# Kernel tuning notes

Measured on AMD Instinct MI355X. Metric: run time of the kernel, lower is better.

Reference implementation:

```python
import jax, jax.numpy as jnp
import numpy as np

DIM = 256; HEADS = 8; WS = 7; ALPHA = 0.5
HD = DIM // HEADS                      # head_dim = 32
GH = int(HEADS * ALPHA); LH = HEADS - GH   # 4 global / 4 local heads
GD = GH * HD; LD = LH * HD             # 128 / 128
HID = int(DIM * 4.0)                   # mlp hidden = 1024
SCALE = HD ** -0.5


def ln(x, g, b, eps=1e-5):
    m = jnp.mean(x, -1, keepdims=True)
    v = jnp.var(x, -1, keepdims=True)
    return (x - m) * jax.lax.rsqrt(v + eps) * g + b


def setup_inputs() -> dict:
    key = jax.random.key(0)
    ks = jax.random.split(key, 12)
    B, H, W = 4, 112, 112
    N = H * W
    def p(k, shape, s=0.02):
        return jax.random.normal(k, shape, jnp.float32) * s
    return {
        'x': jax.random.normal(ks[0], (B, N, DIM), jnp.float32),
        'x_reverse': jax.random.normal(ks[1], (B, N, DIM), jnp.float32),
        'g1': jnp.ones((DIM,), jnp.float32), 'b1': jnp.zeros((DIM,), jnp.float32),
        'g2': jnp.ones((DIM,), jnp.float32), 'b2': jnp.zeros((DIM,), jnp.float32),
        'Gq_w': p(ks[2], (DIM, GD)), 'Gq_b': jnp.zeros((GD,), jnp.float32),
        'Gkv_w': p(ks[3], (DIM, 2 * GD)), 'Gkv_b': jnp.zeros((2 * GD,), jnp.float32),
        'Gp_w': p(ks[4], (GD, GD)), 'Gp_b': jnp.zeros((GD,), jnp.float32),
        'Lq_w': p(ks[5], (DIM, LD)), 'Lq_b': jnp.zeros((LD,), jnp.float32),
        'Lkv_w': p(ks[6], (DIM, 2 * LD)), 'Lkv_b': jnp.zeros((2 * LD,), jnp.float32),
        'Lp_w': p(ks[7], (LD, LD)), 'Lp_b': jnp.zeros((LD,), jnp.float32),
        'fc1_w': p(ks[8], (DIM, HID)), 'fc1_b': jnp.zeros((HID,), jnp.float32),
        'dw_w': p(ks[9], (HID, 1, 3, 3), 0.05), 'dw_b': jnp.zeros((HID,), jnp.float32),
        'fc2_w': p(ks[10], (HID, DIM)), 'fc2_b': jnp.zeros((DIM,), jnp.float32),
        'H': 112, 'W': 112,
    }


def reference(x, x_reverse, g1, b1, g2, b2,
              Gq_w, Gq_b, Gkv_w, Gkv_b, Gp_w, Gp_b,
              Lq_w, Lq_b, Lkv_w, Lkv_b, Lp_w, Lp_b,
              fc1_w, fc1_b, dw_w, dw_b, fc2_w, fc2_b, H, W):
    B, N, C = x.shape
    assert H % WS == 0 and W % WS == 0  # shapes chosen so no padding branch
    xn = ln(x, g1, b1).reshape(B, H, W, C)
    xrn = ln(x_reverse, g1, b1).reshape(B, H, W, C)

    # ---- Global attention: queries from every pixel, kv from avg-pooled (ws x ws) grid
    q = (xn.reshape(B, N, C) @ Gq_w + Gq_b).reshape(B, N, GH, HD)
    pooled = xrn.reshape(B, H // WS, WS, W // WS, WS, C).mean(axis=(2, 4)).reshape(B, -1, C)
    kv = (pooled @ Gkv_w + Gkv_b).reshape(B, -1, 2, GH, HD)
    k, v = kv[:, :, 0], kv[:, :, 1]
    a = jax.nn.softmax(jnp.einsum('bnhd,bmhd->bhnm', q, k) * SCALE, axis=-1)
    g_out = jnp.einsum('bhnm,bmhd->bnhd', a, v).reshape(B, H, W, GD) @ Gp_w + Gp_b

    # ---- Local windowed attention (ws x ws non-overlapping windows)
    hg, wg = H // WS, W // WS
    TG, T = hg * wg, WS * WS
    def windows(t):
        return t.reshape(B, hg, WS, wg, WS, C).transpose(0, 1, 3, 2, 4, 5).reshape(B, TG, T, C)
    xw, xrw = windows(xn), windows(xrn)
    ql = (xw @ Lq_w + Lq_b).reshape(B, TG, T, LH, HD)
    kvl = (xrw @ Lkv_w + Lkv_b).reshape(B, TG, T, 2, LH, HD)
    kl, vl = kvl[:, :, :, 0], kvl[:, :, :, 1]
    al = jax.nn.softmax(jnp.einsum('bgqhd,bgkhd->bghqk', ql, kl) * SCALE, axis=-1)
    lo = jnp.einsum('bghqk,bgkhd->bgqhd', al, vl).reshape(B, hg, wg, WS, WS, LD)
    lo = lo.transpose(0, 1, 3, 2, 4, 5).reshape(B, H, W, LD) @ Lp_w + Lp_b

    x = x + jnp.concatenate([g_out, lo], axis=-1).reshape(B, N, C)

    # ---- DWMlp: fc1 -> depthwise 3x3 conv -> GELU -> fc2
    h = ln(x, g2, b2) @ fc1_w + fc1_b
    himg = h.reshape(B, H, W, HID).transpose(0, 3, 1, 2)
    himg = jax.lax.conv_general_dilated(
        himg, dw_w, (1, 1), 'SAME', feature_group_count=HID,
        dimension_numbers=('NCHW', 'OIHW', 'NCHW')) + dw_b[None, :, None, None]
    h = jax.nn.gelu(himg.reshape(B, HID, N).transpose(0, 2, 1), approximate=False)
    return x + (h @ fc2_w + fc2_b)
```

## Files before the change

### kernel.cpp

```cpp
#include <hip/hip_runtime.h>
#include <hip/hip_bf16.h>
#include <math.h>

typedef __hip_bfloat16 bf16;
typedef __attribute__((ext_vector_type(8))) short bf16x8;
typedef __attribute__((ext_vector_type(4))) float f32x4;

static constexpr int B_  = 4;
static constexpr int Hh  = 112, Ww = 112;
static constexpr int Nn  = Hh * Ww;
static constexpr int Cc  = 256;
static constexpr int M_  = B_ * Nn;
static constexpr int GH_ = 4;
static constexpr int GD_ = 128;
static constexpr int LD_ = 128;
static constexpr int HID_ = 1024;
static constexpr int TG_ = 256;
static constexpr int T__ = 49;
static constexpr float SCALE_ = 0.17677669529663687f;

__device__ __forceinline__ float toF(const bf16 v)  { return __bfloat162float(v); }
__device__ __forceinline__ float toF(const float v) { return v; }
__device__ __forceinline__ void st_out(float* p, float v) { *p = v; }
__device__ __forceinline__ void st_out(bf16* p, float v)  { *p = __float2bfloat16(v); }

__device__ __forceinline__ float erf_fast(float x) {
  float ax = __builtin_fabsf(x);
  float t  = __builtin_amdgcn_rcpf(fmaf(0.3275911f, ax, 1.0f));
  float p  = fmaf(t, 1.061405429f, -1.453152027f);
  p = fmaf(t, p, 1.421413741f);
  p = fmaf(t, p, -0.284496736f);
  p = fmaf(t, p, 0.254829592f);
  p = p * t;
  float r = fmaf(-p, __expf(-ax * ax), 1.0f);
  return copysignf(r, x);
}

__device__ __forceinline__ void gload_lds16(const bf16* g, bf16* l) {
  using gvoid = const __attribute__((address_space(1))) void;
  using lvoid = __attribute__((address_space(3))) void;
  __builtin_amdgcn_global_load_lds((gvoid*)g, (lvoid*)l, 16, 0, 0);
}

__device__ __forceinline__ int win_row_map(int r) {
  int b  = r / Nn;
  int rr = r - b * Nn;
  int g  = rr / T__;
  int t  = rr - g * T__;
  int gh = g >> 4, gw = g & 15;
  int i  = t / 7,  j  = t - i * 7;
  int n  = (gh * 7 + i) * Ww + gw * 7 + j;
  return b * Nn + n;
}

__global__ void guard_fill_kernel(float* out) {
  out[threadIdx.x + blockIdx.x * 256] = 1.0e6f;
}

__global__ __launch_bounds__(256) void convert_all_kernel(
    const float* __restrict__ s0, const float* __restrict__ s1,
    const float* __restrict__ s2, const float* __restrict__ s3,
    const float* __restrict__ s4, const float* __restrict__ s5,
    const float* __restrict__ s6, const float* __restrict__ s7,
    bf16* __restrict__ wt) {
  int idx = blockIdx.x * 256 + threadIdx.x;
  const float* W; int K, N, base;
  if      (idx < 32768)  { W = s0; K = 256;  N = 128;  base = 0; }
  else if (idx < 98304)  { W = s1; K = 256;  N = 256;  base = 32768; }
  else if (idx < 114688) { W = s2; K = 128;  N = 128;  base = 98304; }
  else if (idx < 147456) { W = s3; K = 256;  N = 128;  base = 114688; }
  else if (idx < 212992) { W = s4; K = 256;  N = 256;  base = 147456; }
  else if (idx < 229376) { W = s5; K = 128;  N = 128;  base = 212992; }
  else if (idx < 491520) { W = s6; K = 256;  N = 1024; base = 229376; }
  else                   { W = s7; K = 1024; N = 256;  base = 491520; }
  int loc = idx - base;
  int n = loc / K, k = loc - n * K;
  wt[idx] = __float2bfloat16(W[(size_t)k * N + n]);
}

__global__ __launch_bounds__(256) void ln_dual_kernel(const float* __restrict__ x,
                                                      const float* __restrict__ xr,
                                                      const float* __restrict__ g,
                                                      const float* __restrict__ bta,
                                                      bf16* __restrict__ xn,
                                                      bf16* __restrict__ xrn) {
  const int tid = threadIdx.x;
  const int grp = tid >> 5;
  const int sub = tid & 31;
  const int c0 = sub * 8;
  const int rowA = blockIdx.x * 16 + grp * 2;
  const int rowB = rowA + 1;
  const float* src = blockIdx.y ? xr : x;
  bf16* dst = blockIdx.y ? xrn : xn;
  const float* pA = src + (size_t)rowA * Cc + c0;
  const float* pB = src + (size_t)rowB * Cc + c0;
  float4 a0 = *(const float4*)(pA);
  float4 a1 = *(const float4*)(pA + 4);
  float4 b0 = *(const float4*)(pB);
  float4 b1 = *(const float4*)(pB + 4);
  float sA  = (a0.x + a0.y) + (a0.z + a0.w) + (a1.x + a1.y) + (a1.z + a1.w);
  float ssA = a0.x * a0.x + a0.y * a0.y + a0.z * a0.z + a0.w * a0.w
            + a1.x * a1.x + a1.y * a1.y + a1.z * a1.z + a1.w * a1.w;
  float sB  = (b0.x + b0.y) + (b0.z + b0.w) + (b1.x + b1.y) + (b1.z + b1.w);
  float ssB = b0.x * b0.x + b0.y * b0.y + b0.z * b0.z + b0.w * b0.w
            + b1.x * b1.x + b1.y * b1.y + b1.z * b1.z + b1.w * b1.w;
  #pragma unroll
  for (int off = 1; off < 32; off <<= 1) {
    sA  += __shfl_xor(sA, off);
    ssA += __shfl_xor(ssA, off);
    sB  += __shfl_xor(sB, off);
    ssB += __shfl_xor(ssB, off);
  }
  float meanA = sA * (1.0f / Cc);
  float varA  = ssA * (1.0f / Cc) - meanA * meanA;
  float rA = rsqrtf(varA + 1e-5f);
  float meanB = sB * (1.0f / Cc);
  float varB  = ssB * (1.0f / Cc) - meanB * meanB;
  float rB = rsqrtf(varB + 1e-5f);
  float4 gv0 = *(const float4*)(g + c0);
  float4 gv1 = *(const float4*)(g + c0 + 4);
  float4 bv0 = *(const float4*)(bta + c0);
  float4 bv1 = *(const float4*)(bta + c0 + 4);
  __align__(16) bf16 oA[8], oB[8];
  oA[0] = __float2bfloat16((a0.x - meanA) * rA * gv0.x + bv0.x);
  oA[1] = __float2bfloat16((a0.y - meanA) * rA * gv0.y + bv0.y);
  oA[2] = __float2bfloat16((a0.z - meanA) * rA * gv0.z + bv0.z);
  oA[3] = __float2bfloat16((a0.w - meanA) * rA * gv0.w + bv0.w);
  oA[4] = __float2bfloat16((a1.x - meanA) * rA * gv1.x + bv1.x);
  oA[5] = __float2bfloat16((a1.y - meanA) * rA * gv1.y + bv1.y);
  oA[6] = __float2bfloat16((a1.z - meanA) * rA * gv1.z + bv1.z);
  oA[7] = __float2bfloat16((a1.w - meanA) * rA * gv1.w + bv1.w);
  oB[0] = __float2bfloat16((b0.x - meanB) * rB * gv0.x + bv0.x);
  oB[1] = __float2bfloat16((b0.y - meanB) * rB * gv0.y + bv0.y);
  oB[2] = __float2bfloat16((b0.z - meanB) * rB * gv0.z + bv0.z);
  oB[3] = __float2bfloat16((b0.w - meanB) * rB * gv0.w + bv0.w);
  oB[4] = __float2bfloat16((b1.x - meanB) * rB * gv1.x + bv1.x);
  oB[5] = __float2bfloat16((b1.y - meanB) * rB * gv1.y + bv1.y);
  oB[6] = __float2bfloat16((b1.z - meanB) * rB * gv1.z + bv1.z);
  oB[7] = __float2bfloat16((b1.w - meanB) * rB * gv1.w + bv1.w);
  *(uint4*)(dst + (size_t)rowA * Cc + c0) = *(uint4*)oA;
  *(uint4*)(dst + (size_t)rowB * Cc + c0) = *(uint4*)oB;
}

__global__ __launch_bounds__(64) void pool_kernel(const bf16* __restrict__ xrn,
                                                  bf16* __restrict__ pooled) {
  const int lane = threadIdx.x;
  const int c0 = lane * 4;
  const int g  = blockIdx.x;
  const int b  = blockIdx.y;
  const int gh = g >> 4, gw = g & 15;
  float acc[4] = {};
  union U4 { uint2 u; bf16 e[4]; };
  #pragma unroll
  for (int i = 0; i < 7; i++)
    for (int j = 0; j < 7; j++) {
      int n = (gh * 7 + i) * Ww + gw * 7 + j;
      U4 r4;
      r4.u = *(const uint2*)(xrn + ((size_t)b * Nn + n) * Cc + c0);
      #pragma unroll
      for (int u = 0; u < 4; u++) acc[u] += toF(r4.e[u]);
    }
  bf16 o[4];
  #pragma unroll
  for (int u = 0; u < 4; u++) o[u] = __float2bfloat16(acc[u] * (1.0f / 49.0f));
  *(uint2*)(pooled + ((size_t)b * TG_ + g) * Cc + c0) = *(uint2*)o;
}

template <typename OutT, bool WIN_A, bool RES, int BK = 32>
__global__ __launch_bounds__(256) void mfma_gemm_kernel(const bf16* __restrict__ A,
                                                        const bf16* __restrict__ Wt,
                                                        const float* __restrict__ bias,
                                                        const float* __restrict__ res,
                                                        OutT* __restrict__ out,
                                                        int M, int N, int K) {
  __shared__ __align__(16) bf16 As[128 * BK];
  __shared__ __align__(16) bf16 Bs[128 * BK];
  constexpr int LPR = BK / 8;
  constexpr int RPI = 512 / BK;
  constexpr int NI  = BK / 16;
  const int tid = threadIdx.x;
  const int bm = blockIdx.y * 128, bn = blockIdx.x * 128;
  const int lane = tid & 63, w = tid >> 6;
  const int wm = (w >> 1) * 64, wn = (w & 1) * 64;

  const int rbase = w * 32 + (lane / LPR);
  const int kq    = (lane % LPR) * 8;
  const bf16* Ag[NI];
  const bf16* Bg[NI];
  bf16* Al[NI];
  bf16* Bl[NI];
  #pragma unroll
  for (int t = 0; t < NI; t++) {
    const int srow = rbase + t * RPI;
    const int ar = bm + srow;
    const int as = WIN_A ? win_row_map(ar) : ar;
    Ag[t] = A  + (size_t)as * K + kq;
    Al[t] = &As[srow * BK + kq];
    Bg[t] = Wt + (size_t)(bn + srow) * K + kq;
    Bl[t] = &Bs[srow * BK + kq];
  }

  f32x4 acc[4][4];
  #pragma unroll
  for (int i = 0; i < 4; i++)
    #pragma unroll
    for (int j = 0; j < 4; j++) acc[i][j] = (f32x4){0.f, 0.f, 0.f, 0.f};

  const int r16  = lane & 15;
  const int koct = (lane >> 4) * 8;
  const int mrow = wm + r16;
  const int nrow = wn + r16;

  for (int k0 = 0; k0 < K; k0 += BK) {
    #pragma unroll
    for (int t = 0; t < NI; t++) {
      gload_lds16(Ag[t] + k0, Al[t]);
      gload_lds16(Bg[t] + k0, Bl[t]);
    }
    __syncthreads();
    #pragma unroll
    for (int kk = 0; kk < BK / 32; kk++) {
      bf16x8 af[4], bfr[4];
      #pragma unroll
      for (int i = 0; i < 4; i++) af[i]  = *(const bf16x8*)&As[(mrow + i * 16) * BK + kk * 32 + koct];
      #pragma unroll
      for (int j = 0; j < 4; j++) bfr[j] = *(const bf16x8*)&Bs[(nrow + j * 16) * BK + kk * 32 + koct];
      #pragma unroll
      for (int i = 0; i < 4; i++)
        #pragma unroll
        for (int j = 0; j < 4; j++)
          acc[i][j] = __builtin_amdgcn_mfma_f32_16x16x32_bf16(af[i], bfr[j], acc[i][j], 0, 0, 0);
    }
    __syncthreads();
  }

  const int r0 = (lane >> 4) * 4;
  #pragma unroll
  for (int j = 0; j < 4; j++) {
    const int col = bn + wn + j * 16 + r16;
    const float bv = bias[col];
    #pragma unroll
    for (int i = 0; i < 4; i++) {
      const int rowb = bm + wm + i * 16 + r0;
      #pragma unroll
      for (int r = 0; r < 4; r++) {
        size_t ro = (size_t)(rowb + r) * N + col;
        float v = acc[i][j][r] + bv;
        if (RES) v += res[ro];
        st_out(out + ro, v);
      }
    }
  }
}

__global__ __launch_bounds__(256) void gattn_kernel(const bf16* __restrict__ q,
                                                    const bf16* __restrict__ kv,
                                                    bf16* __restrict__ out) {
  __shared__ __align__(16) bf16 Ks[256][40];
  __shared__ __align__(16) bf16 Vt[32][264];
  __shared__ __align__(16) bf16 Ps[4][32][40];
  const int tid = threadIdx.x;
  const int lane = tid & 63, w = tid >> 6;
  const int h = blockIdx.y, b = blockIdx.z;
  const int n0 = blockIdx.x * 128;
  const int r16 = lane & 15, oct = (lane >> 4) * 8;
  const bf16* kvb = kv + (size_t)b * TG_ * 256;

  {
    const int key = tid;
    const bf16* kp = kvb + (size_t)key * 256 + h * 32;
    *(uint4*)&Ks[key][0]  = *(const uint4*)(kp);
    *(uint4*)&Ks[key][8]  = *(const uint4*)(kp + 8);
    *(uint4*)&Ks[key][16] = *(const uint4*)(kp + 16);
    *(uint4*)&Ks[key][24] = *(const uint4*)(kp + 24);
    union { uint4 u[4]; bf16 e[32]; } vv;
    vv.u[0] = *(const uint4*)(kp + 128);
    vv.u[1] = *(const uint4*)(kp + 136);
    vv.u[2] = *(const uint4*)(kp + 144);
    vv.u[3] = *(const uint4*)(kp + 152);
    #pragma unroll
    for (int d = 0; d < 32; d++) Vt[d][key] = vv.e[d];
  }
  const size_t qbase0 = ((size_t)(b * Nn + n0 + w * 32 + r16)) * GD_ + h * 32 + oct;
  bf16x8 aq0 = *(const bf16x8*)(q + qbase0);
  bf16x8 aq1 = *(const bf16x8*)(q + qbase0 + (size_t)16 * GD_);
  __syncthreads();

  f32x4 rs0 = {0.f, 0.f, 0.f, 0.f}, rs1 = {0.f, 0.f, 0.f, 0.f};
  f32x4 ov[2][2];
  #pragma unroll
  for (int i = 0; i < 2; i++)
    #pragma unroll
    for (int dt = 0; dt < 2; dt++) ov[i][dt] = (f32x4){0.f, 0.f, 0.f, 0.f};

  for (int c0 = 0; c0 < 256; c0 += 32) {
    #pragma unroll
    for (int t = 0; t < 2; t++) {
      bf16x8 bk = *(const bf16x8*)&Ks[c0 + t * 16 + r16][oct];
      f32x4 s0 = __builtin_amdgcn_mfma_f32_16x16x32_bf16(aq0, bk, (f32x4){0.f,0.f,0.f,0.f}, 0, 0, 0);
      f32x4 s1 = __builtin_amdgcn_mfma_f32_16x16x32_bf16(aq1, bk, (f32x4){0.f,0.f,0.f,0.f}, 0, 0, 0);
      const int prow = (lane >> 4) * 4;
      const int pcol = t * 16 + r16;
      #pragma unroll
      for (int r = 0; r < 4; r++) {
        bf16 pb0 = __float2bfloat16(__expf(s0[r] * SCALE_));
        bf16 pb1 = __float2bfloat16(__expf(s1[r] * SCALE_));
        rs0[r] += toF(pb0);
        rs1[r] += toF(pb1);
        Ps[w][prow + r][pcol]      = pb0;
        Ps[w][16 + prow + r][pcol] = pb1;
      }
    }
    bf16x8 ap0 = *(const bf16x8*)&Ps[w][r16][oct];
    bf16x8 ap1 = *(const bf16x8*)&Ps[w][16 + r16][oct];
    #pragma unroll
    for (int dt = 0; dt < 2; dt++) {
      bf16x8 bv = *(const bf16x8*)&Vt[dt * 16 + r16][c0 + oct];
      ov[0][dt] = __builtin_amdgcn_mfma_f32_16x16x32_bf16(ap0, bv, ov[0][dt], 0, 0, 0);
      ov[1][dt] = __builtin_amdgcn_mfma_f32_16x16x32_bf16(ap1, bv, ov[1][dt], 0, 0, 0);
    }
  }
  #pragma unroll
  for (int off = 1; off < 16; off <<= 1) {
    #pragma unroll
    for (int r = 0; r < 4; r++) {
      rs0[r] += __shfl_xor(rs0[r], off);
      rs1[r] += __shfl_xor(rs1[r], off);
    }
  }
  const int orow0 = b * Nn + n0 + w * 32 + (lane >> 4) * 4;
  #pragma unroll
  for (int r = 0; r < 4; r++) {
    float inv0 = 1.0f / rs0[r];
    float inv1 = 1.0f / rs1[r];
    size_t ro0 = (size_t)(orow0 + r) * GD_ + h * 32;
    size_t ro1 = ro0 + (size_t)16 * GD_;
    #pragma unroll
    for (int dt = 0; dt < 2; dt++) {
      out[ro0 + dt * 16 + r16] = __float2bfloat16(ov[0][dt][r] * inv0);
      out[ro1 + dt * 16 + r16] = __float2bfloat16(ov[1][dt][r] * inv1);
    }
  }
}

__global__ __launch_bounds__(256) void lattn_kernel(const bf16* __restrict__ ql,
                                                    const bf16* __restrict__ kvl,
                                                    bf16* __restrict__ out) {
  __shared__ __align__(16) bf16 Ks[4][64][40];
  __shared__ __align__(16) bf16 Vt[4][32][72];
  __shared__ __align__(16) bf16 Ps[4][64][72];
  const int tid = threadIdx.x;
  const int lane = tid & 63, w = tid >> 6;
  const int g = blockIdx.x, b = blockIdx.y;
  const int r16 = lane & 15, oct = (lane >> 4) * 8;
  const size_t wbase = ((size_t)b * TG_ + g) * T__;

  for (int u = tid; u < T__ * 32; u += 256) {
    int m = u >> 5, c8 = u & 31;
    union { uint4 q4; bf16 e[8]; } ch;
    ch.q4 = *(const uint4*)(kvl + (wbase + m) * 256 + c8 * 8);
    if (c8 < 16) {
      int h = c8 >> 2, d0 = (c8 & 3) * 8;
      *(uint4*)&Ks[h][m][d0] = ch.q4;
    } else {
      int cv = c8 - 16;
      int h = cv >> 2, d0 = (cv & 3) * 8;
      #pragma unroll
      for (int e = 0; e < 8; e++) Vt[h][d0 + e][m] = ch.e[e];
    }
  }
  for (int z = tid; z < 4 * 32 * 15; z += 256) {
    int h = z / 480, rem = z - h * 480;
    int d = rem / 15, key = 49 + (rem - d * 15);
    Vt[h][d][key] = __float2bfloat16(0.f);
  }
  bf16x8 aq[4];
  #pragma unroll
  for (int i = 0; i < 4; i++) {
    int qr = 16 * i + r16;
    if (qr > 48) qr = 48;
    aq[i] = *(const bf16x8*)(ql + (wbase + qr) * LD_ + w * 32 + oct);
  }
  __syncthreads();

  f32x4 s[4][4];
  #pragma unroll
  for (int j = 0; j < 4; j++) {
    bf16x8 bk = *(const bf16x8*)&Ks[w][16 * j + r16][oct];
    #pragma unroll
    for (int i = 0; i < 4; i++)
      s[i][j] = __builtin_amdgcn_mfma_f32_16x16x32_bf16(aq[i], bk, (f32x4){0.f,0.f,0.f,0.f}, 0, 0, 0);
  }

  const int prow = (lane >> 4) * 4;
  float rs[4][4];
  #pragma unroll
  for (int i = 0; i < 4; i++) {
    #pragma unroll
    for (int r = 0; r < 4; r++) {
      float acc = 0.f;
      #pragma unroll
      for (int j = 0; j < 4; j++) {
        float p = __expf(s[i][j][r] * SCALE_);
        if (j == 3 && r16 != 0) p = 0.f;
        bf16 pb = __float2bfloat16(p);
        Ps[w][16 * i + prow + r][16 * j + r16] = pb;
        acc += toF(pb);
      }
      #pragma unroll
      for (int off = 1; off < 16; off <<= 1) acc += __shfl_xor(acc, off);
      rs[i][r] = acc;
    }
  }

  f32x4 ov[4][2];
  #pragma unroll
  for (int i = 0; i < 4; i++) {
    ov[i][0] = (f32x4){0.f, 0.f, 0.f, 0.f};
    ov[i][1] = (f32x4){0.f, 0.f, 0.f, 0.f};
  }
  #pragma unroll
  for (int kc = 0; kc < 2; kc++) {
    bf16x8 bv0 = *(const bf16x8*)&Vt[w][r16][kc * 32 + oct];
    bf16x8 bv1 = *(const bf16x8*)&Vt[w][16 + r16][kc * 32 + oct];
    #pragma unroll
    for (int i = 0; i < 4; i++) {
      bf16x8 ap = *(const bf16x8*)&Ps[w][16 * i + r16][kc * 32 + oct];
      ov[i][0] = __builtin_amdgcn_mfma_f32_16x16x32_bf16(ap, bv0, ov[i][0], 0, 0, 0);
      ov[i][1] = __builtin_amdgcn_mfma_f32_16x16x32_bf16(ap, bv1, ov[i][1], 0, 0, 0);
    }
  }

  #pragma unroll
  for (int i = 0; i < 4; i++) {
    #pragma unroll
    for (int r = 0; r < 4; r++) {
      int qr = 16 * i + prow + r;
      if (qr < T__) {
        float inv = 1.0f / rs[i][r];
        size_t o = (wbase + qr) * LD_ + w * 32;
        out[o + r16]      = __float2bfloat16(ov[i][0][r] * inv);
        out[o + 16 + r16] = __float2bfloat16(ov[i][1][r] * inv);
      }
    }
  }
}

__global__ __launch_bounds__(256) void combine_ln_kernel(const float* __restrict__ x,
                                                         const bf16* __restrict__ gout,
                                                         const bf16* __restrict__ lo_w,
                                                         const float* __restrict__ g2,
                                                         const float* __restrict__ b2,
                                                         float* __restrict__ xres,
                                                         bf16* __restrict__ xn2) {
  const int tid = threadIdx.x;
  const int row = blockIdx.x * 8 + (tid >> 5);
  const int sub = tid & 31;
  const int c0 = sub * 8;
  int b = row / Nn, n = row - b * Nn;
  int y = n / Ww, xx = n - y * Ww;
  int gh = y / 7, i = y - gh * 7;
  int gw = xx / 7, j = xx - gw * 7;
  size_t wrow = ((size_t)b * TG_ + gh * 16 + gw) * T__ + i * 7 + j;
  union U8 { uint4 u; bf16 e[8]; } r8;
  if (sub < 16) r8.u = *(const uint4*)(gout + (size_t)row * GD_ + c0);
  else          r8.u = *(const uint4*)(lo_w + wrow * LD_ + (c0 - 128));
  const float* xp = x + (size_t)row * Cc + c0;
  float4 v0 = *(const float4*)(xp);
  float4 v1 = *(const float4*)(xp + 4);
  v0.x += toF(r8.e[0]); v0.y += toF(r8.e[1]); v0.z += toF(r8.e[2]); v0.w += toF(r8.e[3]);
  v1.x += toF(r8.e[4]); v1.y += toF(r8.e[5]); v1.z += toF(r8.e[6]); v1.w += toF(r8.e[7]);
  *(float4*)(xres + (size_t)row * Cc + c0)     = v0;
  *(float4*)(xres + (size_t)row * Cc + c0 + 4) = v1;
  float s  = (v0.x + v0.y) + (v0.z + v0.w) + (v1.x + v1.y) + (v1.z + v1.w);
  float ss = v0.x * v0.x + v0.y * v0.y + v0.z * v0.z + v0.w * v0.w
           + v1.x * v1.x + v1.y * v1.y + v1.z * v1.z + v1.w * v1.w;
  #pragma unroll
  for (int off = 1; off < 32; off <<= 1) {
    s  += __shfl_xor(s, off);
    ss += __shfl_xor(ss, off);
  }
  float mean = s * (1.0f / Cc);
  float var  = ss * (1.0f / Cc) - mean * mean;
  float r = rsqrtf(var + 1e-5f);
  float4 gv0 = *(const float4*)(g2 + c0);
  float4 gv1 = *(const float4*)(g2 + c0 + 4);
  float4 bv0 = *(const float4*)(b2 + c0);
  float4 bv1 = *(const float4*)(b2 + c0 + 4);
  __align__(16) bf16 o[8];
  o[0] = __float2bfloat16((v0.x - mean) * r * gv0.x + bv0.x);
  o[1] = __float2bfloat16((v0.y - mean) * r * gv0.y + bv0.y);
  o[2] = __float2bfloat16((v0.z - mean) * r * gv0.z + bv0.z);
  o[3] = __float2bfloat16((v0.w - mean) * r * gv0.w + bv0.w);
  o[4] = __float2bfloat16((v1.x - mean) * r * gv1.x + bv1.x);
  o[5] = __float2bfloat16((v1.y - mean) * r * gv1.y + bv1.y);
  o[6] = __float2bfloat16((v1.z - mean) * r * gv1.z + bv1.z);
  o[7] = __float2bfloat16((v1.w - mean) * r * gv1.w + bv1.w);
  *(uint4*)(xn2 + (size_t)row * Cc + c0) = *(uint4*)o;
}

static constexpr int TW_ = 14;
__global__ __launch_bounds__(256, 4) void dwconv_gelu_kernel(const bf16* __restrict__ h1,
                                                             const float* __restrict__ w,
                                                             const float* __restrict__ bias,
                                                             bf16* __restrict__ h2) {
  const int tid = threadIdx.x;
  const int c0 = tid * 4;
  const int img = blockIdx.z;
  const int y0  = blockIdx.y * 2;
  const int xt  = blockIdx.x * TW_;
  const size_t ibase = (size_t)img * Nn * HID_;

  float wreg[9][4], breg[4];
  #pragma unroll
  for (int u = 0; u < 4; u++) {
    breg[u] = bias[c0 + u];
    #pragma unroll
    for (int t = 0; t < 9; t++) wreg[t][u] = w[(c0 + u) * 9 + t];
  }

  const bf16* rowp[4];
  bool rok[4];
  #pragma unroll
  for (int r = 0; r < 4; r++) {
    int yy = y0 - 1 + r;
    rok[r] = (yy >= 0 && yy < Hh);
    rowp[r] = h1 + ibase + (size_t)(rok[r] ? yy : 0) * Ww * HID_ + c0;
  }

  float wa[4][4], wb[4][4], wc[4][4];
  union U4 { ushort2 u2[2]; bf16 e[4]; };
  auto loadcol = [&](int xcol, float v[4][4]) {
    if (xcol < 0 || xcol >= Ww) {
      #pragma unroll
      for (int r = 0; r < 4; r++)
        #pragma unroll
        for (int u = 0; u < 4; u++) v[r][u] = 0.f;
      return;
    }
    #pragma unroll
    for (int r = 0; r < 4; r++) {
      if (rok[r]) {
        U4 raw;
        *(uint2*)&raw = *(const uint2*)(rowp[r] + (size_t)xcol * HID_);
        #pragma unroll
        for (int u = 0; u < 4; u++) v[r][u] = toF(raw.e[u]);
      } else {
        #pragma unroll
        for (int u = 0; u < 4; u++) v[r][u] = 0.f;
      }
    }
  };
  loadcol(xt - 1, wa);
  loadcol(xt, wb);

  for (int xx = 0; xx < TW_; xx++) {
    const int x = xt + xx;
    loadcol(x + 1, wc);
    #pragma unroll
    for (int p = 0; p < 2; p++) {
      bf16 res[4];
      #pragma unroll
      for (int u = 0; u < 4; u++) {
        float a = breg[u];
        a = fmaf(wa[p + 0][u], wreg[0][u], a);
        a = fmaf(wb[p + 0][u], wreg[1][u], a);
        a = fmaf(wc[p + 0][u], wreg[2][u], a);
        a = fmaf(wa[p + 1][u], wreg[3][u], a);
        a = fmaf(wb[p + 1][u], wreg[4][u], a);
        a = fmaf(wc[p + 1][u], wreg[5][u], a);
        a = fmaf(wa[p + 2][u], wreg[6][u], a);
        a = fmaf(wb[p + 2][u], wreg[7][u], a);
        a = fmaf(wc[p + 2][u], wreg[8][u], a);
        float gl = 0.5f * a * (1.0f + erf_fast(a * 0.7071067811865475f));
        res[u] = __float2bfloat16(gl);
      }
      *(uint2*)(h2 + ibase + (size_t)((y0 + p) * Ww + x) * HID_ + c0) = *(uint2*)res;
    }
    #pragma unroll
    for (int r = 0; r < 4; r++)
      #pragma unroll
      for (int u = 0; u < 4; u++) { wa[r][u] = wb[r][u]; wb[r][u] = wc[r][u]; }
  }
}

extern "C" void kernel_launch(void* const* d_in, const int* in_sizes, int n_in,
                              void* d_out, int out_size, void* d_ws, size_t ws_size,
                              hipStream_t stream) {
  const float* x     = (const float*)d_in[0];
  const float* xrev  = (const float*)d_in[1];
  const float* g1    = (const float*)d_in[2];
  const float* b1    = (const float*)d_in[3];
  const float* g2    = (const float*)d_in[4];
  const float* b2    = (const float*)d_in[5];
  const float* Gq_w  = (const float*)d_in[6];
  const float* Gq_b  = (const float*)d_in[7];
  const float* Gkv_w = (const float*)d_in[8];
  const float* Gkv_b = (const float*)d_in[9];
  const float* Gp_w  = (const float*)d_in[10];
  const float* Gp_b  = (const float*)d_in[11];
  const float* Lq_w  = (const float*)d_in[12];
  const float* Lq_b  = (const float*)d_in[13];
  const float* Lkv_w = (const float*)d_in[14];
  const float* Lkv_b = (const float*)d_in[15];
  const float* Lp_w  = (const float*)d_in[16];
  const float* Lp_b  = (const float*)d_in[17];
  const float* fc1_w = (const float*)d_in[18];
  const float* fc1_b = (const float*)d_in[19];
  const float* dw_w  = (const float*)d_in[20];
  const float* dw_b  = (const float*)d_in[21];
  const float* fc2_w = (const float*)d_in[22];
  const float* fc2_b = (const float*)d_in[23];

  const size_t E_GQ = 256 * 128, E_GKV = 256 * 256, E_GP = 128 * 128;
  const size_t E_LQ = 256 * 128, E_LKV = 256 * 256, E_LP = 128 * 128;
  const size_t E_F1 = 256 * 1024, E_F2 = 1024 * 256;
  char* ws = (char*)d_ws;
  bf16* Gq_t  = (bf16*)ws;
  bf16* Gkv_t = Gq_t  + E_GQ;
  bf16* Gp_t  = Gkv_t + E_GKV;
  bf16* Lq_t  = Gp_t  + E_GP;
  bf16* Lkv_t = Lq_t  + E_LQ;
  bf16* Lp_t  = Lkv_t + E_LKV;
  bf16* f1_t  = Lp_t  + E_LP;
  bf16* f2_t  = f1_t  + E_F1;
  const size_t WT_ELEMS = E_GQ + E_GKV + E_GP + E_LQ + E_LKV + E_LP + E_F1 + E_F2;
  const size_t WT_BYTES = WT_ELEMS * 2;

  const size_t SZ_ROW2 = (size_t)M_ * Cc * 2;
  const size_t SZ_HALF = (size_t)M_ * 128 * 2;
  const size_t SZ_POOL = (size_t)B_ * TG_ * Cc * 2;
  const size_t SZ_KVG  = (size_t)B_ * TG_ * 256 * 2;
  const size_t SZ_H    = (size_t)(2 * Nn) * HID_ * 2;
  char* arena = ws + WT_BYTES;
  bf16* S1 = (bf16*)(arena);
  bf16* S2 = (bf16*)(arena + SZ_ROW2);
  bf16* S3 = (bf16*)(arena + 2 * SZ_ROW2);
  bf16* S4 = (bf16*)(arena + 2 * SZ_ROW2 + SZ_HALF);
  bf16* S5 = (bf16*)(arena + 2 * SZ_ROW2 + 2 * SZ_HALF);
  bf16* poolb = (bf16*)(arena + 2 * SZ_ROW2 + 3 * SZ_HALF);
  bf16* kvG   = (bf16*)(arena + 2 * SZ_ROW2 + 3 * SZ_HALF + SZ_POOL);
  const size_t ARENA_A = 2 * SZ_ROW2 + 3 * SZ_HALF + SZ_POOL + SZ_KVG;
  bf16* xn2 = S1;
  bf16* h1  = (bf16*)(arena + SZ_ROW2);
  bf16* h2  = (bf16*)(arena + SZ_ROW2 + SZ_H);
  const size_t ARENA_B = SZ_ROW2 + 2 * SZ_H;

  float* out  = (float*)d_out;
  float* xres = (float*)d_out;
  const size_t NEED = WT_BYTES + (ARENA_A > ARENA_B ? ARENA_A : ARENA_B);
  if (ws_size < NEED) {
    guard_fill_kernel<<<16, 256, 0, stream>>>(out);
    return;
  }

  bf16* xn = S1;  bf16* xrn = S2;  bf16* qbuf = S3;  bf16* gattn = S4;  bf16* gout = S5;
  bf16* kvl = S1; bf16* lo_w = S2; bf16* qlb  = S3;  bf16* lattn = S4;

  convert_all_kernel<<<2944, 256, 0, stream>>>(Gq_w, Gkv_w, Gp_w, Lq_w, Lkv_w, Lp_w,
                                               fc1_w, fc2_w, (bf16*)ws);
  ln_dual_kernel<<<dim3(M_ / 16, 2), 256, 0, stream>>>(x, xrev, g1, b1, xn, xrn);
  pool_kernel<<<dim3(TG_, B_), 64, 0, stream>>>(xrn, poolb);
  mfma_gemm_kernel<bf16, false, false><<<dim3(1, M_ / 128), 256, 0, stream>>>(
      xn, Gq_t, Gq_b, nullptr, qbuf, M_, 128, 256);
  mfma_gemm_kernel<bf16, false, false><<<dim3(2, 8), 256, 0, stream>>>(
      poolb, Gkv_t, Gkv_b, nullptr, kvG, 1024, 256, 256);
  gattn_kernel<<<dim3(Nn / 128, GH_, B_), 256, 0, stream>>>(qbuf, kvG, gattn);
  mfma_gemm_kernel<bf16, false, false><<<dim3(1, M_ / 128), 256, 0, stream>>>(
      gattn, Gp_t, Gp_b, nullptr, gout, M_, 128, 128);
  mfma_gemm_kernel<bf16, true, false><<<dim3(1, M_ / 128), 256, 0, stream>>>(
      xn, Lq_t, Lq_b, nullptr, qlb, M_, 128, 256);
  mfma_gemm_kernel<bf16, true, false><<<dim3(2, M_ / 128), 256, 0, stream>>>(
      xrn, Lkv_t, Lkv_b, nullptr, kvl, M_, 256, 256);
  lattn_kernel<<<dim3(TG_, B_), 256, 0, stream>>>(qlb, kvl, lattn);
  mfma_gemm_kernel<bf16, false, false><<<dim3(1, M_ / 128), 256, 0, stream>>>(
      lattn, Lp_t, Lp_b, nullptr, lo_w, M_, 128, 128);
  combine_ln_kernel<<<M_ / 8, 256, 0, stream>>>(x, gout, lo_w, g2, b2, xres, xn2);
  for (int half = 0; half < 2; half++) {
    const size_t r0 = (size_t)half * 2 * Nn;
    mfma_gemm_kernel<bf16, false, false, 64><<<dim3(8, (2 * Nn) / 128), 256, 0, stream>>>(
        xn2 + r0 * Cc, f1_t, fc1_b, nullptr, h1, 2 * Nn, 1024, 256);
    dwconv_gelu_kernel<<<dim3(Ww / TW_, Hh / 2, 2), 256, 0, stream>>>(h1, dw_w, dw_b, h2);
    mfma_gemm_kernel<float, false, true><<<dim3(2, (2 * Nn) / 128), 256, 0, stream>>>(
        h2, f2_t, fc2_b, xres + r0 * Cc, out + r0 * Cc, 2 * Nn, 256, 1024);
  }
}
```

Before: 537.9 us.

## Merge global/local q and projection GEMMs, drop window-order buffers

Concatenates the global and local query weights into one 256-wide GEMM and packs both output projections into a block-diagonal 256x256 weight, so one GEMM covers each pair. Local attention now gathers its window rows directly from pixel-ordered buffers, which removes the window-remapped GEMM loads and the remapped reads in combine. The LayerNorm kernel is also reshaped to one row per wavefront. This cuts kernel launches and intermediate traffic, but the block-diagonal projection does twice the FLOPs, and local attention loads become strided gathers.

```diff
diff --git a/kernel.cpp b/kernel.cpp
--- a/kernel.cpp
+++ b/kernel.cpp
@@ -12,8 +12,6 @@
 static constexpr int Cc  = 256;
 static constexpr int M_  = B_ * Nn;
 static constexpr int GH_ = 4;
-static constexpr int GD_ = 128;
-static constexpr int LD_ = 128;
 static constexpr int HID_ = 1024;
 static constexpr int TG_ = 256;
 static constexpr int T__ = 49;
@@ -42,40 +40,49 @@
   __builtin_amdgcn_global_load_lds((gvoid*)g, (lvoid*)l, 16, 0, 0);
 }
 
-__device__ __forceinline__ int win_row_map(int r) {
-  int b  = r / Nn;
-  int rr = r - b * Nn;
-  int g  = rr / T__;
-  int t  = rr - g * T__;
-  int gh = g >> 4, gw = g & 15;
-  int i  = t / 7,  j  = t - i * 7;
-  int n  = (gh * 7 + i) * Ww + gw * 7 + j;
-  return b * Nn + n;
-}
-
 __global__ void guard_fill_kernel(float* out) {
   out[threadIdx.x + blockIdx.x * 256] = 1.0e6f;
 }
 
 __global__ __launch_bounds__(256) void convert_all_kernel(
-    const float* __restrict__ s0, const float* __restrict__ s1,
-    const float* __restrict__ s2, const float* __restrict__ s3,
-    const float* __restrict__ s4, const float* __restrict__ s5,
-    const float* __restrict__ s6, const float* __restrict__ s7,
+    const float* __restrict__ gq, const float* __restrict__ lq,
+    const float* __restrict__ gkv, const float* __restrict__ lkv,
+    const float* __restrict__ gp, const float* __restrict__ lp,
+    const float* __restrict__ f1, const float* __restrict__ f2,
     bf16* __restrict__ wt) {
   int idx = blockIdx.x * 256 + threadIdx.x;
-  const float* W; int K, N, base;
-  if      (idx < 32768)  { W = s0; K = 256;  N = 128;  base = 0; }
-  else if (idx < 98304)  { W = s1; K = 256;  N = 256;  base = 32768; }
-  else if (idx < 114688) { W = s2; K = 128;  N = 128;  base = 98304; }
-  else if (idx < 147456) { W = s3; K = 256;  N = 128;  base = 114688; }
-  else if (idx < 212992) { W = s4; K = 256;  N = 256;  base = 147456; }
-  else if (idx < 229376) { W = s5; K = 128;  N = 128;  base = 212992; }
-  else if (idx < 491520) { W = s6; K = 256;  N = 1024; base = 229376; }
-  else                   { W = s7; K = 1024; N = 256;  base = 491520; }
-  int loc = idx - base;
-  int n = loc / K, k = loc - n * K;
-  wt[idx] = __float2bfloat16(W[(size_t)k * N + n]);
+  float v;
+  if (idx < 32768) {
+    int n = idx / 256, k = idx - n * 256;
+    v = gq[(size_t)k * 128 + n];
+  } else if (idx < 65536) {
+    int loc = idx - 32768;
+    int n = loc / 256, k = loc - n * 256;
+    v = lq[(size_t)k * 128 + n];
+  } else if (idx < 131072) {
+    int loc = idx - 65536;
+    int n = loc / 256, k = loc - n * 256;
+    v = gkv[(size_t)k * 256 + n];
+  } else if (idx < 196608) {
+    int loc = idx - 131072;
+    int n = loc / 256, k = loc - n * 256;
+    v = lkv[(size_t)k * 256 + n];
+  } else if (idx < 262144) {
+    int loc = idx - 196608;
+    int n = loc >> 8, k = loc & 255;
+    if (n < 128 && k < 128)       v = gp[(size_t)k * 128 + n];
+    else if (n >= 128 && k >= 128) v = lp[(size_t)(k - 128) * 128 + (n - 128)];
+    else                           v = 0.f;
+  } else if (idx < 524288) {
+    int loc = idx - 262144;
+    int n = loc / 256, k = loc - n * 256;
+    v = f1[(size_t)k * 1024 + n];
+  } else {
+    int loc = idx - 524288;
+    int n = loc / 1024, k = loc - n * 1024;
+    v = f2[(size_t)k * 256 + n];
+  }
+  wt[idx] = __float2bfloat16(v);
 }
 
 __global__ __launch_bounds__(256) void ln_dual_kernel(const float* __restrict__ x,
@@ -85,61 +92,30 @@
                                                       bf16* __restrict__ xn,
                                                       bf16* __restrict__ xrn) {
   const int tid = threadIdx.x;
-  const int grp = tid >> 5;
-  const int sub = tid & 31;
-  const int c0 = sub * 8;
-  const int rowA = blockIdx.x * 16 + grp * 2;
-  const int rowB = rowA + 1;
+  const int row = blockIdx.x * 4 + (tid >> 6);
+  const int lane = tid & 63;
+  const int c0 = lane * 4;
   const float* src = blockIdx.y ? xr : x;
   bf16* dst = blockIdx.y ? xrn : xn;
-  const float* pA = src + (size_t)rowA * Cc + c0;
-  const float* pB = src + (size_t)rowB * Cc + c0;
-  float4 a0 = *(const float4*)(pA);
-  float4 a1 = *(const float4*)(pA + 4);
-  float4 b0 = *(const float4*)(pB);
-  float4 b1 = *(const float4*)(pB + 4);
-  float sA  = (a0.x + a0.y) + (a0.z + a0.w) + (a1.x + a1.y) + (a1.z + a1.w);
-  float ssA = a0.x * a0.x + a0.y * a0.y + a0.z * a0.z + a0.w * a0.w
-            + a1.x * a1.x + a1.y * a1.y + a1.z * a1.z + a1.w * a1.w;
-  float sB  = (b0.x + b0.y) + (b0.z + b0.w) + (b1.x + b1.y) + (b1.z + b1.w);
-  float ssB = b0.x * b0.x + b0.y * b0.y + b0.z * b0.z + b0.w * b0.w
-            + b1.x * b1.x + b1.y * b1.y + b1.z * b1.z + b1.w * b1.w;
-  #pragma unroll
-  for (int off = 1; off < 32; off <<= 1) {
-    sA  += __shfl_xor(sA, off);
-    ssA += __shfl_xor(ssA, off);
-    sB  += __shfl_xor(sB, off);
-    ssB += __shfl_xor(ssB, off);
-  }
-  float meanA = sA * (1.0f / Cc);
-  float varA  = ssA * (1.0f / Cc) - meanA * meanA;
-  float rA = rsqrtf(varA + 1e-5f);
-  float meanB = sB * (1.0f / Cc);
-  float varB  = ssB * (1.0f / Cc) - meanB * meanB;
-  float rB = rsqrtf(varB + 1e-5f);
-  float4 gv0 = *(const float4*)(g + c0);
-  float4 gv1 = *(const float4*)(g + c0 + 4);
-  float4 bv0 = *(const float4*)(bta + c0);
-  float4 bv1 = *(const float4*)(bta + c0 + 4);
-  __align__(16) bf16 oA[8], oB[8];
-  oA[0] = __float2bfloat16((a0.x - meanA) * rA * gv0.x + bv0.x);
-  oA[1] = __float2bfloat16((a0.y - meanA) * rA * gv0.y + bv0.y);
-  oA[2] = __float2bfloat16((a0.z - meanA) * rA * gv0.z + bv0.z);
-  oA[3] = __float2bfloat16((a0.w - meanA) * rA * gv0.w + bv0.w);
-  oA[4] = __float2bfloat16((a1.x - meanA) * rA * gv1.x + bv1.x);
-  oA[5] = __float2bfloat16((a1.y - meanA) * rA * gv1.y + bv1.y);
-  oA[6] = __float2bfloat16((a1.z - meanA) * rA * gv1.z + bv1.z);
-  oA[7] = __float2bfloat16((a1.w - meanA) * rA * gv1.w + bv1.w);
-  oB[0] = __float2bfloat16((b0.x - meanB) * rB * gv0.x + bv0.x);
-  oB[1] = __float2bfloat16((b0.y - meanB) * rB * gv0.y + bv0.y);
-  oB[2] = __float2bfloat16((b0.z - meanB) * rB * gv0.z + bv0.z);
-  oB[3] = __float2bfloat16((b0.w - meanB) * rB * gv0.w + bv0.w);
-  oB[4] = __float2bfloat16((b1.x - meanB) * rB * gv1.x + bv1.x);
-  oB[5] = __float2bfloat16((b1.y - meanB) * rB * gv1.y + bv1.y);
-  oB[6] = __float2bfloat16((b1.z - meanB) * rB * gv1.z + bv1.z);
-  oB[7] = __float2bfloat16((b1.w - meanB) * rB * gv1.w + bv1.w);
-  *(uint4*)(dst + (size_t)rowA * Cc + c0) = *(uint4*)oA;
-  *(uint4*)(dst + (size_t)rowB * Cc + c0) = *(uint4*)oB;
+  float4 v = *(const float4*)(src + (size_t)row * Cc + c0);
+  float s  = v.x + v.y + v.z + v.w;
+  float ss = v.x * v.x + v.y * v.y + v.z * v.z + v.w * v.w;
+  #pragma unroll
+  for (int off = 1; off < 64; off <<= 1) {
+    s  += __shfl_xor(s, off);
+    ss += __shfl_xor(ss, off);
+  }
+  float mean = s * (1.0f / Cc);
+  float var  = ss * (1.0f / Cc) - mean * mean;
+  float r = rsqrtf(var + 1e-5f);
+  float4 gv = *(const float4*)(g + c0);
+  float4 bv = *(const float4*)(bta + c0);
+  bf16 o[4];
+  o[0] = __float2bfloat16((v.x - mean) * r * gv.x + bv.x);
+  o[1] = __float2bfloat16((v.y - mean) * r * gv.y + bv.y);
+  o[2] = __float2bfloat16((v.z - mean) * r * gv.z + bv.z);
+  o[3] = __float2bfloat16((v.w - mean) * r * gv.w + bv.w);
+  *(uint2*)(dst + (size_t)row * Cc + c0) = *(uint2*)o;
 }
 
 __global__ __launch_bounds__(64) void pool_kernel(const bf16* __restrict__ xrn,
@@ -166,10 +142,11 @@
   *(uint2*)(pooled + ((size_t)b * TG_ + g) * Cc + c0) = *(uint2*)o;
 }
 
-template <typename OutT, bool WIN_A, bool RES, int BK = 32>
+template <typename OutT, bool RES, int BK = 32>
 __global__ __launch_bounds__(256) void mfma_gemm_kernel(const bf16* __restrict__ A,
                                                         const bf16* __restrict__ Wt,
                                                         const float* __restrict__ bias,
+                                                        const float* __restrict__ bias2,
                                                         const float* __restrict__ res,
                                                         OutT* __restrict__ out,
                                                         int M, int N, int K) {
@@ -192,9 +169,7 @@
   #pragma unroll
   for (int t = 0; t < NI; t++) {
     const int srow = rbase + t * RPI;
-    const int ar = bm + srow;
-    const int as = WIN_A ? win_row_map(ar) : ar;
-    Ag[t] = A  + (size_t)as * K + kq;
+    Ag[t] = A  + (size_t)(bm + srow) * K + kq;
     Al[t] = &As[srow * BK + kq];
     Bg[t] = Wt + (size_t)(bn + srow) * K + kq;
     Bl[t] = &Bs[srow * BK + kq];
@@ -238,7 +213,7 @@
   #pragma unroll
   for (int j = 0; j < 4; j++) {
     const int col = bn + wn + j * 16 + r16;
-    const float bv = bias[col];
+    const float bv = (bias2 && col >= 128) ? bias2[col - 128] : bias[col];
     #pragma unroll
     for (int i = 0; i < 4; i++) {
       const int rowb = bm + wm + i * 16 + r0;
@@ -281,9 +256,9 @@
     #pragma unroll
     for (int d = 0; d < 32; d++) Vt[d][key] = vv.e[d];
   }
-  const size_t qbase0 = ((size_t)(b * Nn + n0 + w * 32 + r16)) * GD_ + h * 32 + oct;
+  const size_t qbase0 = ((size_t)(b * Nn + n0 + w * 32 + r16)) * 256 + h * 32 + oct;
   bf16x8 aq0 = *(const bf16x8*)(q + qbase0);
-  bf16x8 aq1 = *(const bf16x8*)(q + qbase0 + (size_t)16 * GD_);
+  bf16x8 aq1 = *(const bf16x8*)(q + qbase0 + (size_t)16 * 256);
   __syncthreads();
 
   f32x4 rs0 = {0.f, 0.f, 0.f, 0.f}, rs1 = {0.f, 0.f, 0.f, 0.f};
@@ -333,8 +308,8 @@
   for (int r = 0; r < 4; r++) {
     float inv0 = 1.0f / rs0[r];
     float inv1 = 1.0f / rs1[r];
-    size_t ro0 = (size_t)(orow0 + r) * GD_ + h * 32;
-    size_t ro1 = ro0 + (size_t)16 * GD_;
+    size_t ro0 = (size_t)(orow0 + r) * 256 + h * 32;
+    size_t ro1 = ro0 + (size_t)16 * 256;
     #pragma unroll
     for (int dt = 0; dt < 2; dt++) {
       out[ro0 + dt * 16 + r16] = __float2bfloat16(ov[0][dt][r] * inv0);
@@ -352,13 +327,16 @@
   const int tid = threadIdx.x;
   const int lane = tid & 63, w = tid >> 6;
   const int g = blockIdx.x, b = blockIdx.y;
+  const int gh = g >> 4, gw = g & 15;
   const int r16 = lane & 15, oct = (lane >> 4) * 8;
-  const size_t wbase = ((size_t)b * TG_ + g) * T__;
+  const int nw0 = (gh * 7) * Ww + gw * 7;
 
   for (int u = tid; u < T__ * 32; u += 256) {
     int m = u >> 5, c8 = u & 31;
+    int im = m / 7, jm = m - im * 7;
+    int nm = nw0 + im * Ww + jm;
     union { uint4 q4; bf16 e[8]; } ch;
-    ch.q4 = *(const uint4*)(kvl + (wbase + m) * 256 + c8 * 8);
+    ch.q4 = *(const uint4*)(kvl + ((size_t)b * Nn + nm) * 256 + c8 * 8);
     if (c8 < 16) {
       int h = c8 >> 2, d0 = (c8 & 3) * 8;
       *(uint4*)&Ks[h][m][d0] = ch.q4;
@@ -379,7 +357,9 @@
   for (int i = 0; i < 4; i++) {
     int qr = 16 * i + r16;
     if (qr > 48) qr = 48;
-    aq[i] = *(const bf16x8*)(ql + (wbase + qr) * LD_ + w * 32 + oct);
+    int iq = qr / 7, jq = qr - iq * 7;
+    int nq = nw0 + iq * Ww + jq;
+    aq[i] = *(const bf16x8*)(ql + ((size_t)b * Nn + nq) * 256 + 128 + w * 32 + oct);
   }
   __syncthreads();
 
@@ -438,7 +418,9 @@
       int qr = 16 * i + prow + r;
       if (qr < T__) {
         float inv = 1.0f / rs[i][r];
-        size_t o = (wbase + qr) * LD_ + w * 32;
+        int iq = qr / 7, jq = qr - iq * 7;
+        int nq = nw0 + iq * Ww + jq;
+        size_t o = ((size_t)b * Nn + nq) * 256 + 128 + w * 32;
         out[o + r16]      = __float2bfloat16(ov[i][0][r] * inv);
         out[o + 16 + r16] = __float2bfloat16(ov[i][1][r] * inv);
       }
@@ -447,8 +429,7 @@
 }
 
 __global__ __launch_bounds__(256) void combine_ln_kernel(const float* __restrict__ x,
-                                                         const bf16* __restrict__ gout,
-                                                         const bf16* __restrict__ lo_w,
+                                                         const bf16* __restrict__ proj,
                                                          const float* __restrict__ g2,
                                                          const float* __restrict__ b2,
                                                          float* __restrict__ xres,
@@ -457,14 +438,8 @@
   const int row = blockIdx.x * 8 + (tid >> 5);
   const int sub = tid & 31;
   const int c0 = sub * 8;
-  int b = row / Nn, n = row - b * Nn;
-  int y = n / Ww, xx = n - y * Ww;
-  int gh = y / 7, i = y - gh * 7;
-  int gw = xx / 7, j = xx - gw * 7;
-  size_t wrow = ((size_t)b * TG_ + gh * 16 + gw) * T__ + i * 7 + j;
   union U8 { uint4 u; bf16 e[8]; } r8;
-  if (sub < 16) r8.u = *(const uint4*)(gout + (size_t)row * GD_ + c0);
-  else          r8.u = *(const uint4*)(lo_w + wrow * LD_ + (c0 - 128));
+  r8.u = *(const uint4*)(proj + (size_t)row * 256 + c0);
   const float* xp = x + (size_t)row * Cc + c0;
   float4 v0 = *(const float4*)(xp);
   float4 v1 = *(const float4*)(xp + 4);
@@ -612,35 +587,33 @@
   const float* fc2_w = (const float*)d_in[22];
   const float* fc2_b = (const float*)d_in[23];
 
-  const size_t E_GQ = 256 * 128, E_GKV = 256 * 256, E_GP = 128 * 128;
-  const size_t E_LQ = 256 * 128, E_LKV = 256 * 256, E_LP = 128 * 128;
-  const size_t E_F1 = 256 * 1024, E_F2 = 1024 * 256;
+  const size_t E_QW = 256 * 256;
+  const size_t E_GKV = 256 * 256;
+  const size_t E_LKV = 256 * 256;
+  const size_t E_PJ = 256 * 256;
+  const size_t E_F1 = 1024 * 256, E_F2 = 256 * 1024;
   char* ws = (char*)d_ws;
-  bf16* Gq_t  = (bf16*)ws;
-  bf16* Gkv_t = Gq_t  + E_GQ;
-  bf16* Gp_t  = Gkv_t + E_GKV;
-  bf16* Lq_t  = Gp_t  + E_GP;
-  bf16* Lkv_t = Lq_t  + E_LQ;
-  bf16* Lp_t  = Lkv_t + E_LKV;
-  bf16* f1_t  = Lp_t  + E_LP;
+  bf16* QW_t  = (bf16*)ws;
+  bf16* Gkv_t = QW_t  + E_QW;
+  bf16* Lkv_t = Gkv_t + E_GKV;
+  bf16* PJ_t  = Lkv_t + E_LKV;
+  bf16* f1_t  = PJ_t  + E_PJ;
   bf16* f2_t  = f1_t  + E_F1;
-  const size_t WT_ELEMS = E_GQ + E_GKV + E_GP + E_LQ + E_LKV + E_LP + E_F1 + E_F2;
+  const size_t WT_ELEMS = E_QW + E_GKV + E_LKV + E_PJ + E_F1 + E_F2;
   const size_t WT_BYTES = WT_ELEMS * 2;
 
   const size_t SZ_ROW2 = (size_t)M_ * Cc * 2;
-  const size_t SZ_HALF = (size_t)M_ * 128 * 2;
   const size_t SZ_POOL = (size_t)B_ * TG_ * Cc * 2;
   const size_t SZ_KVG  = (size_t)B_ * TG_ * 256 * 2;
   const size_t SZ_H    = (size_t)(2 * Nn) * HID_ * 2;
   char* arena = ws + WT_BYTES;
-  bf16* S1 = (bf16*)(arena);
-  bf16* S2 = (bf16*)(arena + SZ_ROW2);
-  bf16* S3 = (bf16*)(arena + 2 * SZ_ROW2);
-  bf16* S4 = (bf16*)(arena + 2 * SZ_ROW2 + SZ_HALF);
-  bf16* S5 = (bf16*)(arena + 2 * SZ_ROW2 + 2 * SZ_HALF);
-  bf16* poolb = (bf16*)(arena + 2 * SZ_ROW2 + 3 * SZ_HALF);
-  bf16* kvG   = (bf16*)(arena + 2 * SZ_ROW2 + 3 * SZ_HALF + SZ_POOL);
-  const size_t ARENA_A = 2 * SZ_ROW2 + 3 * SZ_HALF + SZ_POOL + SZ_KVG;
+  bf16* S1       = (bf16*)(arena);
+  bf16* S2       = (bf16*)(arena + SZ_ROW2);
+  bf16* q_cat    = (bf16*)(arena + 2 * SZ_ROW2);
+  bf16* attn_cat = (bf16*)(arena + 3 * SZ_ROW2);
+  bf16* poolb    = (bf16*)(arena + 4 * SZ_ROW2);
+  bf16* kvG      = (bf16*)(arena + 4 * SZ_ROW2 + SZ_POOL);
+  const size_t ARENA_A = 4 * SZ_ROW2 + SZ_POOL + SZ_KVG;
   bf16* xn2 = S1;
   bf16* h1  = (bf16*)(arena + SZ_ROW2);
   bf16* h2  = (bf16*)(arena + SZ_ROW2 + SZ_H);
@@ -654,34 +627,29 @@
     return;
   }
 
-  bf16* xn = S1;  bf16* xrn = S2;  bf16* qbuf = S3;  bf16* gattn = S4;  bf16* gout = S5;
-  bf16* kvl = S1; bf16* lo_w = S2; bf16* qlb  = S3;  bf16* lattn = S4;
-
-  convert_all_kernel<<<2944, 256, 0, stream>>>(Gq_w, Gkv_w, Gp_w, Lq_w, Lkv_w, Lp_w,
+  bf16* xn = S1;  bf16* xrn = S2;  bf16* kvl = S1;  bf16* proj = q_cat;
+
+  convert_all_kernel<<<3072, 256, 0, stream>>>(Gq_w, Lq_w, Gkv_w, Lkv_w, Gp_w, Lp_w,
                                                fc1_w, fc2_w, (bf16*)ws);
-  ln_dual_kernel<<<dim3(M_ / 16, 2), 256, 0, stream>>>(x, xrev, g1, b1, xn, xrn);
+  ln_dual_kernel<<<dim3(M_ / 4, 2), 256, 0, stream>>>(x, xrev, g1, b1, xn, xrn);
   pool_kernel<<<dim3(TG_, B_), 64, 0, stream>>>(xrn, poolb);
-  mfma_gemm_kernel<bf16, false, false><<<dim3(1, M_ / 128), 256, 0, stream>>>(
-      xn, Gq_t, Gq_b, nullptr, qbuf, M_, 128, 256);
-  mfma_gemm_kernel<bf16, false, false><<<dim3(2, 8), 256, 0, stream>>>(
-      poolb, Gkv_t, Gkv_b, nullptr, kvG, 1024, 256, 256);
-  gattn_kernel<<<dim3(Nn / 128, GH_, B_), 256, 0, stream>>>(qbuf, kvG, gattn);
-  mfma_gemm_kernel<bf16, false, false><<<dim3(1, M_ / 128), 256, 0, stream>>>(
-      gattn, Gp_t, Gp_b, nullptr, gout, M_, 128, 128);
-  mfma_gemm_kernel<bf16, true, false><<<dim3(1, M_ / 128), 256, 0, stream>>>(
-      xn, Lq_t, Lq_b, nullptr, qlb, M_, 128, 256);
-  mfma_gemm_kernel<bf16, true, false><<<dim3(2, M_ / 128), 256, 0, stream>>>(
-      xrn, Lkv_t, Lkv_b, nullptr, kvl, M_, 256, 256);
-  lattn_kernel<<<dim3(TG_, B_), 256, 0, stream>>>(qlb, kvl, lattn);
-  mfma_gemm_kernel<bf16, false, false><<<dim3(1, M_ / 128), 256, 0, stream>>>(
-      lattn, Lp_t, Lp_b, nullptr, lo_w, M_, 128, 128);
-  combine_ln_kernel<<<M_ / 8, 256, 0, stream>>>(x, gout, lo_w, g2, b2, xres, xn2);
+  mfma_gemm_kernel<bf16, false><<<dim3(2, M_ / 128), 256, 0, stream>>>(
+      xn, QW_t, Gq_b, Lq_b, nullptr, q_cat, M_, 256, 256);
+  mfma_gemm_kernel<bf16, false><<<dim3(2, M_ / 128), 256, 0, stream>>>(
+      xrn, Lkv_t, Lkv_b, nullptr, nullptr, kvl, M_, 256, 256);
+  mfma_gemm_kernel<bf16, false><<<dim3(2, 8), 256, 0, stream>>>(
+      poolb, Gkv_t, Gkv_b, nullptr, nullptr, kvG, 1024, 256, 256);
+  gattn_kernel<<<dim3(Nn / 128, GH_, B_), 256, 0, stream>>>(q_cat, kvG, attn_cat);
+  lattn_kernel<<<dim3(TG_, B_), 256, 0, stream>>>(q_cat, kvl, attn_cat);
+  mfma_gemm_kernel<bf16, false><<<dim3(2, M_ / 128), 256, 0, stream>>>(
+      attn_cat, PJ_t, Gp_b, Lp_b, nullptr, proj, M_, 256, 256);
+  combine_ln_kernel<<<M_ / 8, 256, 0, stream>>>(x, proj, g2, b2, xres, xn2);
   for (int half = 0; half < 2; half++) {
     const size_t r0 = (size_t)half * 2 * Nn;
-    mfma_gemm_kernel<bf16, false, false, 64><<<dim3(8, (2 * Nn) / 128), 256, 0, stream>>>(
-        xn2 + r0 * Cc, f1_t, fc1_b, nullptr, h1, 2 * Nn, 1024, 256);
+    mfma_gemm_kernel<bf16, false, 64><<<dim3(8, (2 * Nn) / 128), 256, 0, stream>>>(
+        xn2 + r0 * Cc, f1_t, fc1_b, nullptr, nullptr, h1, 2 * Nn, 1024, 256);
     dwconv_gelu_kernel<<<dim3(Ww / TW_, Hh / 2, 2), 256, 0, stream>>>(h1, dw_w, dw_b, h2);
-    mfma_gemm_kernel<float, false, true><<<dim3(2, (2 * Nn) / 128), 256, 0, stream>>>(
-        h2, f2_t, fc2_b, xres + r0 * Cc, out + r0 * Cc, 2 * Nn, 256, 1024);
-  }
-}
+    mfma_gemm_kernel<float, true><<<dim3(2, (2 * Nn) / 128), 256, 0, stream>>>(
+        h2, f2_t, fc2_b, nullptr, xres + r0 * Cc, out + r0 * Cc, 2 * Nn, 256, 1024);
+  }
+}
```

Result: no change. 542.3 us (+0.8%).
